# Kernel optimization log

Hardware: AMD Instinct MI355X
Metric: run time of the kernel (lower is better)

Reference implementation:

```python
import jax, jax.numpy as jnp
import numpy as np

N = 100000      # nodes
E = 3200000     # edges (avg degree 32)
NODE, EDGE, H = 11, 2, 32
EPS = 1e-5


def setup_inputs() -> dict:
    key = jax.random.key(0)
    ks = jax.random.split(key, 12)
    def w(k, shape):  # small init like torch Linear
        return jax.random.normal(k, shape, dtype=jnp.float32) * 0.1
    inp = {
        'x': jax.random.normal(ks[0], (N, NODE), dtype=jnp.float32),
        'edge_attr': jax.random.normal(ks[1], (E, EDGE), dtype=jnp.float32),
        'edge_index': jax.random.randint(ks[2], (2, E), 0, N),
        # mlp1: Lin(13,32)-BN-ReLU-Lin(32,32)-BN-ReLU
        'w1a': w(ks[3], (NODE + EDGE, H)), 'b1a': jnp.zeros(H), 'g1a': jnp.ones(H), 'be1a': jnp.zeros(H),
        'w1b': w(ks[4], (H, H)),           'b1b': jnp.zeros(H), 'g1b': jnp.ones(H), 'be1b': jnp.zeros(H),
        # mlp2: Lin(43,32)-BN-ReLU then Lin(32,1)-ReLU (no BN on last)
        'w2a': w(ks[5], (NODE + H, H)), 'b2a': jnp.zeros(H), 'g2a': jnp.ones(H), 'be2a': jnp.zeros(H),
        'w2b': w(ks[6], (H, 1)),        'b2b': jnp.zeros(1),
        # power: Lin(11,32)-BN-ReLU-Lin(32,1)-BN-ReLU
        'wpa': w(ks[7], (NODE, H)), 'bpa': jnp.zeros(H), 'gpa': jnp.ones(H), 'bepa': jnp.zeros(H),
        'wpb': w(ks[8], (H, 1)),    'bpb': jnp.zeros(1), 'gpb': jnp.ones(1), 'bepb': jnp.zeros(1),
    }
    return inp


def _bn(x, g, b):
    # training-mode BatchNorm1d (batch stats, biased variance), like torch default
    mu = x.mean(0, keepdims=True)
    var = ((x - mu) ** 2).mean(0, keepdims=True)
    return (x - mu) * jax.lax.rsqrt(var + EPS) * g + b


def _conv(x, edge_index, edge_attr,
          w1a, b1a, g1a, be1a, w1b, b1b, g1b, be1b,
          w2a, b2a, g2a, be2a, w2b, b2b):
    src, dst = edge_index[0], edge_index[1]
    # message: cat([x_j, edge_attr]) -> mlp1
    m = jnp.concatenate([x[src], edge_attr], axis=1)          # [E, 13]
    m = jax.nn.relu(_bn(m @ w1a + b1a, g1a, be1a))            # [E, 32]
    m = jax.nn.relu(_bn(m @ w1b + b1b, g1b, be1b))            # [E, 32]
    # aggr='max' scatter to destination nodes
    agg = jax.ops.segment_max(m, dst, num_segments=x.shape[0])
    agg = jnp.where(jnp.isneginf(agg), 0.0, agg)              # empty segments -> 0
    # update: cat([x, aggr_out]) -> mlp2, then replace last feature column
    h = jax.nn.relu(_bn(jnp.concatenate([x, agg], axis=1) @ w2a + b2a, g2a, be2a))
    comb = jax.nn.relu(h @ w2b + b2b)                         # [N, 1]
    return jnp.concatenate([x[:, :-1], comb], axis=1)         # [N, 11]


def reference(x, edge_attr, edge_index,
              w1a, b1a, g1a, be1a, w1b, b1b, g1b, be1b,
              w2a, b2a, g2a, be2a, w2b, b2b,
              wpa, bpa, gpa, bepa, wpb, bpb, gpb, bepb):
    for _ in range(3):
        x = _conv(x, edge_index, edge_attr,
                  w1a, b1a, g1a, be1a, w1b, b1b, g1b, be1b,
                  w2a, b2a, g2a, be2a, w2b, b2b)
    h = jax.nn.relu(_bn(x @ wpa + bpa, gpa, bepa))
    out = jax.nn.relu(_bn(h @ wpb + bpb, gpb, bepb))
    return out
```

## Files before the change

### kernel.cpp

```cpp
#include <hip/hip_runtime.h>
#include <hip/hip_bf16.h>
#include <cstddef>

#define NN 100000
#define EE 3200000
#define NBIN 64
static const float EF = 3200000.0f;
#define INVN (1.0f / 100000.0f)

typedef __attribute__((ext_vector_type(8))) short bf16x8;
typedef __attribute__((ext_vector_type(16))) float f32x16;


__device__ __forceinline__ float wsum(float v) {
  #pragma unroll
  for (int off = 32; off > 0; off >>= 1) v += __shfl_down(v, off, 64);
  return v;
}

__device__ __forceinline__ void reduce64(float sum[32], float ssq[32], float* red,
                                         float* __restrict__ gsum, float* __restrict__ gssq) {
  const int wid = threadIdx.x >> 6, lane = threadIdx.x & 63;
  #pragma unroll
  for (int j = 0; j < 32; j++) {
    float a = wsum(sum[j]);
    float b = wsum(ssq[j]);
    if (lane == 0) { red[wid * 64 + j] = a; red[wid * 64 + 32 + j] = b; }
  }
  __syncthreads();
  if (threadIdx.x < 64) {
    float t = red[threadIdx.x] + red[64 + threadIdx.x] + red[128 + threadIdx.x] + red[192 + threadIdx.x];
    if (threadIdx.x < 32) unsafeAtomicAdd(&gsum[threadIdx.x], t);
    else                  unsafeAtomicAdd(&gssq[threadIdx.x - 32], t);
  }
}

__device__ __forceinline__ void loadrow(const float* __restrict__ xp, int s, float in[13]) {
  const float4* xr = reinterpret_cast<const float4*>(xp + (size_t)s * 12);
  float4 r0 = xr[0], r1 = xr[1], r2 = xr[2];
  in[0]=r0.x; in[1]=r0.y; in[2]=r0.z; in[3]=r0.w; in[4]=r1.x; in[5]=r1.y; in[6]=r1.z; in[7]=r1.w;
  in[8]=r2.x; in[9]=r2.y; in[10]=r2.z;
}

__device__ __forceinline__ unsigned long long packsea(float x, float y) {
  unsigned int xq = (unsigned int)(fmaf(x, 16384.f, 131072.f) + 0.5f);
  unsigned int yq = (unsigned int)(fmaf(y, 16384.f, 131072.f) + 0.5f);
  return (1ULL << 54) | ((unsigned long long)yq << 27) | (unsigned long long)xq;
}

__device__ __forceinline__ short tobf(float f) {
  return (short)((__float_as_uint(f) + 0x8000u) >> 16);
}
__device__ __forceinline__ float bfhi(float f) {
  return __uint_as_float(__float_as_uint(f) & 0xFFFF0000u);
}
__device__ __forceinline__ short bfhi_s(float f) {
  return (short)(__float_as_uint(f) >> 16);
}


__global__ __launch_bounds__(256) void k_wprep(const float* __restrict__ w1b,
    const float* __restrict__ b1b, const float* __restrict__ g1b,
    const float* __restrict__ w2a, const float* __restrict__ b2a,
    const float* __restrict__ wpa, const float* __restrict__ bpa,
    float* __restrict__ w2tf, float* __restrict__ b1bf,
    float* __restrict__ w2aT, float* __restrict__ wpaT) {
  int t = threadIdx.x;
  for (int i = t; i < 1024; i += 256) {
    int j = i >> 5, k = i & 31;
    float d = (g1b[j] >= 0.f) ? 1.f : -1.f;
    w2tf[j * 32 + k] = d * w1b[k * 32 + j];
  }
  for (int i = t; i < 32 * 43; i += 256) { int j = i & 31, k = i >> 5; w2aT[j * 44 + k] = w2a[k * 32 + j]; }
  for (int i = t; i < 32 * 11; i += 256) { int j = i & 31, k = i >> 5; wpaT[j * 12 + k] = wpa[k * 32 + j]; }
  if (t < 32) {
    float d = (g1b[t] >= 0.f) ? 1.f : -1.f;
    b1bf[t] = d * b1b[t];
    w2aT[t * 44 + 43] = b2a[t];
    wpaT[t * 12 + 11] = bpa[t];
  }
}

__global__ __launch_bounds__(256) void k_prep(const int* __restrict__ dst, const int* __restrict__ src,
    const float* __restrict__ ea, int* __restrict__ cnt, int* __restrict__ rank,
    unsigned long long* __restrict__ nsd, float* __restrict__ cmom) {
  float p0 = 0, p1 = 0, p2 = 0, p3 = 0, p4 = 0;
  const int S = gridDim.x * 256;
  for (int g = blockIdx.x * 256 + threadIdx.x; g < EE / 4; g += S) {
    int4 d4 = reinterpret_cast<const int4*>(dst)[g];
    int4 s4 = reinterpret_cast<const int4*>(src)[g];
    float4 e0 = reinterpret_cast<const float4*>(ea)[2 * g];
    float4 e1 = reinterpret_cast<const float4*>(ea)[2 * g + 1];
    int r0 = atomicAdd(&cnt[d4.x], 1);
    int r1 = atomicAdd(&cnt[d4.y], 1);
    int r2 = atomicAdd(&cnt[d4.z], 1);
    int r3 = atomicAdd(&cnt[d4.w], 1);
    reinterpret_cast<int4*>(rank)[g] = make_int4(r0, r1, r2, r3);
    atomicAdd(&nsd[s4.x], packsea(e0.x, e0.y));
    atomicAdd(&nsd[s4.y], packsea(e0.z, e0.w));
    atomicAdd(&nsd[s4.z], packsea(e1.x, e1.y));
    atomicAdd(&nsd[s4.w], packsea(e1.z, e1.w));
    p0 += e0.x * e0.x + e0.z * e0.z + e1.x * e1.x + e1.z * e1.z;
    p1 += e0.x * e0.y + e0.z * e0.w + e1.x * e1.y + e1.z * e1.w;
    p2 += e0.y * e0.y + e0.w * e0.w + e1.y * e1.y + e1.w * e1.w;
    p3 += e0.x + e0.z + e1.x + e1.z;
    p4 += e0.y + e0.w + e1.y + e1.w;
  }
  p0 = wsum(p0); p1 = wsum(p1); p2 = wsum(p2); p3 = wsum(p3); p4 = wsum(p4);
  if ((threadIdx.x & 63) == 0) {
    unsafeAtomicAdd(&cmom[0], p0); unsafeAtomicAdd(&cmom[1], p1); unsafeAtomicAdd(&cmom[2], p2);
    unsafeAtomicAdd(&cmom[3], p3); unsafeAtomicAdd(&cmom[4], p4);
  }
}

__global__ __launch_bounds__(1024) void k_scan(const int* __restrict__ cnt,
                                               int* __restrict__ starts) {
  __shared__ int part[1024];
  const int T = 1024, CH = (NN + T - 1) / T;
  int t = threadIdx.x;
  int lo = t * CH, hi = min(lo + CH, NN);
  int s = 0;
  for (int i = lo; i < hi; i++) s += cnt[i];
  part[t] = s; __syncthreads();
  for (int off = 1; off < T; off <<= 1) {
    int v = (t >= off) ? part[t - off] : 0;
    __syncthreads();
    part[t] += v;
    __syncthreads();
  }
  int run = part[t] - s;
  for (int i = lo; i < hi; i++) { starts[i] = run; run += cnt[i]; }
  if (t == T - 1) starts[NN] = EE;
}

__global__ __launch_bounds__(256) void k_scatter(const int* __restrict__ dst, const int* __restrict__ src,
    const float* __restrict__ ea, const int* __restrict__ starts, const int* __restrict__ rank,
    int4* __restrict__ edg) {
  const int S = gridDim.x * 256;
  for (int g = blockIdx.x * 256 + threadIdx.x; g < EE / 4; g += S) {
    int4 d4 = reinterpret_cast<const int4*>(dst)[g];
    int4 s4 = reinterpret_cast<const int4*>(src)[g];
    int4 r4 = reinterpret_cast<const int4*>(rank)[g];
    float4 e0 = reinterpret_cast<const float4*>(ea)[2 * g];
    float4 e1 = reinterpret_cast<const float4*>(ea)[2 * g + 1];
    edg[starts[d4.x] + r4.x] = make_int4(s4.x, __float_as_int(e0.x), __float_as_int(e0.y), 0);
    edg[starts[d4.y] + r4.y] = make_int4(s4.y, __float_as_int(e0.z), __float_as_int(e0.w), 0);
    edg[starts[d4.z] + r4.z] = make_int4(s4.z, __float_as_int(e1.x), __float_as_int(e1.y), 0);
    edg[starts[d4.w] + r4.w] = make_int4(s4.w, __float_as_int(e1.z), __float_as_int(e1.w), 0);
  }
}

__global__ __launch_bounds__(256) void k_xp(const float* __restrict__ x, float* __restrict__ xp) {
  int n = blockIdx.x * 256 + threadIdx.x;
  if (n >= NN) return;
  float v[11];
  #pragma unroll
  for (int k = 0; k < 11; k++) v[k] = x[(size_t)n * 11 + k];
  float4* o = reinterpret_cast<float4*>(xp + (size_t)n * 12);
  o[0] = make_float4(v[0], v[1], v[2], v[3]);
  o[1] = make_float4(v[4], v[5], v[6], v[7]);
  o[2] = make_float4(v[8], v[9], v[10], 0.f);
}

__global__ __launch_bounds__(256) void k_mom(const float* __restrict__ xp,
                                             const unsigned long long* __restrict__ nsd,
                                             float* __restrict__ mom) {
  const int n = blockIdx.x * 256 + threadIdx.x;
  const int lane = threadIdx.x & 63;
  float v[11]; float w = 0.f; float sx = 0.f, sy = 0.f;
  #pragma unroll
  for (int k = 0; k < 11; k++) v[k] = 0.f;
  if (n < NN) {
    unsigned long long pv = nsd[n];
    float dg = (float)(unsigned int)(pv >> 54);
    float sxf = (float)(unsigned int)(pv & 0x7FFFFFFull);
    float syf = (float)(unsigned int)((pv >> 27) & 0x7FFFFFFull);
    w = dg;
    sx = sxf * (1.f / 16384.f) - 8.f * dg;
    sy = syf * (1.f / 16384.f) - 8.f * dg;
    loadrow(xp, n, v);
  }
  int ch = 0;
  #pragma unroll
  for (int a = 0; a < 11; a++) {
    float r = wsum(w * v[a]);
    if (lane == 0) unsafeAtomicAdd(&mom[ch], r);
    ch++;
  }
  #pragma unroll
  for (int a = 0; a < 11; a++) {
    #pragma unroll
    for (int b = a; b < 11; b++) {
      float r = wsum(w * v[a] * v[b]);
      if (lane == 0) unsafeAtomicAdd(&mom[ch], r);
      ch++;
    }
  }
  #pragma unroll
  for (int a = 0; a < 11; a++) {
    float rx = wsum(v[a] * sx);
    if (lane == 0) unsafeAtomicAdd(&mom[ch], rx);
    ch++;
    float ry = wsum(v[a] * sy);
    if (lane == 0) unsafeAtomicAdd(&mom[ch], ry);
    ch++;
  }
}

__device__ __forceinline__ float msym(const float* mom, const float* cmom, int k, int l) {
  int a = min(k, l), b = max(k, l);
  if (b < 11) return mom[11 + a * 11 - a * (a - 1) / 2 + (b - a)];
  if (a < 11) return mom[77 + a * 2 + (b - 11)];
  return cmom[(a - 11) + (b - 11)];
}

__global__ __launch_bounds__(256) void k_P(const float* __restrict__ xp,
    const float* __restrict__ mom, const float* __restrict__ cmom,
    const float* __restrict__ w1a, const float* __restrict__ b1a,
    const float* __restrict__ g1a, const float* __restrict__ be1a,
    float* __restrict__ wexy, float* __restrict__ statsbase, float* __restrict__ P) {
  __shared__ float w1fs[32 * 14];
  const int t = threadIdx.x;
  if (t < 32) {
    const int jj = t;
    float w[13], S[13];
    #pragma unroll
    for (int k = 0; k < 13; k++) w[k] = w1a[k * 32 + jj];
    #pragma unroll
    for (int k = 0; k < 11; k++) S[k] = mom[k];
    S[11] = cmom[3]; S[12] = cmom[4];
    float lin = 0.f;
    #pragma unroll
    for (int k = 0; k < 13; k++) lin = fmaf(w[k], S[k], lin);
    float quad = 0.f;
    #pragma unroll
    for (int k = 0; k < 13; k++)
      #pragma unroll
      for (int l = 0; l < 13; l++) quad = fmaf(w[k] * w[l], msym(mom, cmom, k, l), quad);
    const float invE = 1.f / EF;
    float b = b1a[jj];
    float mean = fmaf(lin, invE, b);
    float ey2 = (quad + 2.f * b * lin) * invE + b * b;
    float var = fmaxf(ey2 - mean * mean, 0.f);
    float A = g1a[jj] * rsqrtf(var + 1e-5f);
    float C = be1a[jj] - mean * A;
    #pragma unroll
    for (int k = 0; k < 11; k++) w1fs[jj * 14 + k] = A * w[k];
    w1fs[jj * 14 + 11] = 0.f; w1fs[jj * 14 + 12] = 0.f;
    w1fs[jj * 14 + 13] = fmaf(A, b, C);
    if (blockIdx.x == 0) { wexy[jj] = A * w[11]; wexy[32 + jj] = A * w[12]; }
  }
  if (blockIdx.x == 0 && t >= 64 && t < 128) statsbase[t] = 0.f;
  __syncthreads();
  const int n = blockIdx.x * 256 + t;
  if (n >= NN) return;
  float xv[11];
  loadrow(xp, n, xv);
  float4* op = reinterpret_cast<float4*>(P + (size_t)n * 32);
  #pragma unroll
  for (int jj = 0; jj < 8; jj++) {
    float o[4];
    #pragma unroll
    for (int u = 0; u < 4; u++) {
      int j = 4 * jj + u;
      const float* wr = w1fs + j * 14;
      float acc = wr[13];
      #pragma unroll
      for (int k = 0; k < 11; k++) acc = fmaf(xv[k], wr[k], acc);
      o[u] = acc;
    }
    op[jj] = make_float4(o[0], o[1], o[2], o[3]);
  }
}

__global__ __launch_bounds__(256, 4) void k_fusedagg(
    const int* __restrict__ starts, const int4* __restrict__ edg,
    const float* __restrict__ P, const float* __restrict__ wexy,
    const float* __restrict__ w2tf, const float* __restrict__ b1bf,
    float* __restrict__ tzb, float* __restrict__ gms, float* __restrict__ gzq) {
  const int tid = threadIdx.x;
  const int wid = tid >> 6, lane = tid & 63;
  const int j = lane & 31;
  const int h = lane >> 5;
  const int k1 = 8 * h;
  const int k2 = 16 + 8 * h;
  float wexk[16], weyk[16];
  #pragma unroll
  for (int i = 0; i < 8; i++) {
    wexk[i]     = wexy[k1 + i];  weyk[i]     = wexy[32 + k1 + i];
    wexk[8 + i] = wexy[k2 + i];  weyk[8 + i] = wexy[32 + k2 + i];
  }
  bf16x8 B1h, B1l, B2h, B2l;
  #pragma unroll
  for (int i = 0; i < 8; i++) {
    float w1 = w2tf[j * 32 + k1 + i];
    B1h[i] = bfhi_s(w1); B1l[i] = tobf(w1 - bfhi(w1));
    float w2 = w2tf[j * 32 + k2 + i];
    B2h[i] = bfhi_s(w2); B2l[i] = tobf(w2 - bfhi(w2));
  }
  const float bz = b1bf[j];
  float ms[16];
  #pragma unroll
  for (int i = 0; i < 16; i++) ms[i] = 0.f;
  float zq = 0.f;
  const int nwaves = gridDim.x * 4;
  for (int n = blockIdx.x * 4 + wid; n < NN; n += nwaves) {
    const int lo = starts[n], hi = starts[n + 1];
    float tzn = -3.0e38f;
    for (int base = lo; base < hi; base += 32) {
      const int v = min(hi - base, 32);
      const bool ev = j < v;
      const int4 r = edg[ev ? (base + j) : (hi - 1)];
      const float ex = __int_as_float(r.y), ey = __int_as_float(r.z);
      const float* pr = P + (size_t)r.x * 32;
      const float4 p0 = *reinterpret_cast<const float4*>(pr + k1);
      const float4 p1 = *reinterpret_cast<const float4*>(pr + k1 + 4);
      const float4 p2 = *reinterpret_cast<const float4*>(pr + k2);
      const float4 p3 = *reinterpret_cast<const float4*>(pr + k2 + 4);
      const float vm = ev ? 1.f : 0.f;
      float mv[16];
      mv[0]  = vm * fmaxf(0.f, fmaf(ex, wexk[0],  fmaf(ey, weyk[0],  p0.x)));
      mv[1]  = vm * fmaxf(0.f, fmaf(ex, wexk[1],  fmaf(ey, weyk[1],  p0.y)));
      mv[2]  = vm * fmaxf(0.f, fmaf(ex, wexk[2],  fmaf(ey, weyk[2],  p0.z)));
      mv[3]  = vm * fmaxf(0.f, fmaf(ex, wexk[3],  fmaf(ey, weyk[3],  p0.w)));
      mv[4]  = vm * fmaxf(0.f, fmaf(ex, wexk[4],  fmaf(ey, weyk[4],  p1.x)));
      mv[5]  = vm * fmaxf(0.f, fmaf(ex, wexk[5],  fmaf(ey, weyk[5],  p1.y)));
      mv[6]  = vm * fmaxf(0.f, fmaf(ex, wexk[6],  fmaf(ey, weyk[6],  p1.z)));
      mv[7]  = vm * fmaxf(0.f, fmaf(ex, wexk[7],  fmaf(ey, weyk[7],  p1.w)));
      mv[8]  = vm * fmaxf(0.f, fmaf(ex, wexk[8],  fmaf(ey, weyk[8],  p2.x)));
      mv[9]  = vm * fmaxf(0.f, fmaf(ex, wexk[9],  fmaf(ey, weyk[9],  p2.y)));
      mv[10] = vm * fmaxf(0.f, fmaf(ex, wexk[10], fmaf(ey, weyk[10], p2.z)));
      mv[11] = vm * fmaxf(0.f, fmaf(ex, wexk[11], fmaf(ey, weyk[11], p2.w)));
      mv[12] = vm * fmaxf(0.f, fmaf(ex, wexk[12], fmaf(ey, weyk[12], p3.x)));
      mv[13] = vm * fmaxf(0.f, fmaf(ex, wexk[13], fmaf(ey, weyk[13], p3.y)));
      mv[14] = vm * fmaxf(0.f, fmaf(ex, wexk[14], fmaf(ey, weyk[14], p3.z)));
      mv[15] = vm * fmaxf(0.f, fmaf(ex, wexk[15], fmaf(ey, weyk[15], p3.w)));
      #pragma unroll
      for (int i = 0; i < 16; i++) ms[i] += mv[i];
      bf16x8 A1h, A1l, A2h, A2l;
      #pragma unroll
      for (int i = 0; i < 8; i++) {
        A1h[i] = bfhi_s(mv[i]);     A1l[i] = tobf(mv[i] - bfhi(mv[i]));
        A2h[i] = bfhi_s(mv[8 + i]); A2l[i] = tobf(mv[8 + i] - bfhi(mv[8 + i]));
      }
      f32x16 acc;
      #pragma unroll
      for (int i = 0; i < 16; i++) acc[i] = 0.f;
      acc = __builtin_amdgcn_mfma_f32_32x32x16_bf16(A1h, B1h, acc, 0, 0, 0);
      acc = __builtin_amdgcn_mfma_f32_32x32x16_bf16(A1h, B1l, acc, 0, 0, 0);
      acc = __builtin_amdgcn_mfma_f32_32x32x16_bf16(A1l, B1h, acc, 0, 0, 0);
      acc = __builtin_amdgcn_mfma_f32_32x32x16_bf16(A2h, B2h, acc, 0, 0, 0);
      acc = __builtin_amdgcn_mfma_f32_32x32x16_bf16(A2h, B2l, acc, 0, 0, 0);
      acc = __builtin_amdgcn_mfma_f32_32x32x16_bf16(A2l, B2h, acc, 0, 0, 0);
      const int rb = base + 4 * h;
      #pragma unroll
      for (int rg = 0; rg < 16; rg++) {
        const int row = (rg & 3) + 8 * (rg >> 2);
        const bool rv = (rb + row) < hi;
        const float z = acc[rg] + bz;
        tzn = fmaxf(tzn, rv ? z : -3.0e38f);
        const float zz = rv ? z : 0.f;
        zq = fmaf(zz, zz, zq);
      }
    }
    tzn = fmaxf(tzn, __shfl_xor(tzn, 32, 64));
    if (lane < 32) tzb[(size_t)n * 32 + j] = tzn;
  }
  const int bin = blockIdx.x & (NBIN - 1);
  float zqT = zq + __shfl_xor(zq, 32, 64);
  if (lane < 32) unsafeAtomicAdd(&gzq[bin * 32 + j], zqT);
  #pragma unroll
  for (int i = 0; i < 16; i++) {
    ms[i] += __shfl_xor(ms[i], 16, 64);
    ms[i] += __shfl_xor(ms[i], 8, 64);
    ms[i] += __shfl_xor(ms[i], 4, 64);
    ms[i] += __shfl_xor(ms[i], 2, 64);
    ms[i] += __shfl_xor(ms[i], 1, 64);
  }
  if (lane == 0) {
    #pragma unroll
    for (int i = 0; i < 8; i++) unsafeAtomicAdd(&gms[bin * 32 + i], ms[i]);
    #pragma unroll
    for (int i = 0; i < 8; i++) unsafeAtomicAdd(&gms[bin * 32 + 16 + i], ms[8 + i]);
  }
  if (lane == 32) {
    #pragma unroll
    for (int i = 0; i < 8; i++) unsafeAtomicAdd(&gms[bin * 32 + 8 + i], ms[i]);
    #pragma unroll
    for (int i = 0; i < 8; i++) unsafeAtomicAdd(&gms[bin * 32 + 24 + i], ms[8 + i]);
  }
}

__global__ __launch_bounds__(256) void k_hpre2(const float* __restrict__ xp,
    const float* __restrict__ tzb, const int* __restrict__ starts,
    const float* __restrict__ gms, const float* __restrict__ gzq,
    const float* __restrict__ w1b, const float* __restrict__ b1b,
    const float* __restrict__ g1b, const float* __restrict__ be1b,
    const float* __restrict__ w2aT,
    float* __restrict__ hpre, float* __restrict__ gsum, float* __restrict__ gssq) {
  __shared__ float red[256], a2s[32], c2s[32], smm[32], szq[32];
  const int t = threadIdx.x;
  if (t < 32) {
    float msj = 0.f, zqj = 0.f;
    for (int b = 0; b < NBIN; b++) { msj += gms[b * 32 + t]; zqj += gzq[b * 32 + t]; }
    smm[t] = msj; szq[t] = zqj;
  }
  __syncthreads();
  if (t < 32) {
    float zs = EF * b1b[t];
    #pragma unroll
    for (int k = 0; k < 32; k++) zs = fmaf(w1b[k * 32 + t], smm[k], zs);
    const float invE = 1.f / EF;
    float mu = zs * invE;
    float var = fmaxf(szq[t] * invE - mu * mu, 0.f);
    float A = g1b[t] * rsqrtf(var + 1e-5f);
    float C = be1b[t] - mu * A;
    float d = (g1b[t] >= 0.f) ? 1.f : -1.f;
    a2s[t] = A * d; c2s[t] = C;
  }
  __syncthreads();
  const int n = blockIdx.x * 256 + t;
  float hh[32], hv[32];
  #pragma unroll
  for (int j = 0; j < 32; j++) hv[j] = 0.f;
  if (n < NN) {
    float xv[11];
    loadrow(xp, n, xv);
    const int dg = starts[n + 1] - starts[n];
    float av[32];
    if (dg > 0) {
      const float4* tp = reinterpret_cast<const float4*>(tzb + (size_t)n * 32);
      #pragma unroll
      for (int j = 0; j < 8; j++) {
        float4 v = tp[j];
        av[4 * j]     = fmaxf(0.f, fmaf(a2s[4 * j],     v.x, c2s[4 * j]));
        av[4 * j + 1] = fmaxf(0.f, fmaf(a2s[4 * j + 1], v.y, c2s[4 * j + 1]));
        av[4 * j + 2] = fmaxf(0.f, fmaf(a2s[4 * j + 2], v.z, c2s[4 * j + 2]));
        av[4 * j + 3] = fmaxf(0.f, fmaf(a2s[4 * j + 3], v.w, c2s[4 * j + 3]));
      }
    } else {
      #pragma unroll
      for (int j = 0; j < 32; j++) av[j] = 0.f;
    }
    #pragma unroll
    for (int j = 0; j < 32; j++) {
      const float* wr = w2aT + j * 44;
      float acc = wr[43];
      #pragma unroll
      for (int k = 0; k < 11; k++) acc = fmaf(xv[k], wr[k], acc);
      #pragma unroll
      for (int k = 0; k < 32; k++) acc = fmaf(av[k], wr[11 + k], acc);
      hv[j] = acc;
    }
    float4* hp = reinterpret_cast<float4*>(hpre + (size_t)n * 32);
    #pragma unroll
    for (int j = 0; j < 8; j++)
      hp[j] = make_float4(hv[4 * j], hv[4 * j + 1], hv[4 * j + 2], hv[4 * j + 3]);
  }
  #pragma unroll
  for (int j = 0; j < 32; j++) hh[j] = hv[j] * hv[j];
  reduce64(hv, hh, red, gsum, gssq);
}

__global__ __launch_bounds__(256) void k_comb(const float* __restrict__ hpre,
    const float* __restrict__ SUM3, const float* __restrict__ SSQ3,
    const float* __restrict__ g2a, const float* __restrict__ be2a,
    const float* __restrict__ w2b, const float* __restrict__ b2b, float* __restrict__ xp,
    float* __restrict__ mom, float* __restrict__ gms, float* __restrict__ gzq) {
  __shared__ float a3s[32], c3s[32];
  const int t = threadIdx.x;
  if (t < 32) {
    float mu = SUM3[t] * INVN;
    float var = fmaxf(SSQ3[t] * INVN - mu * mu, 0.f);
    float s = rsqrtf(var + 1e-5f) * g2a[t];
    a3s[t] = s; c3s[t] = be2a[t] - mu * s;
  }
  __syncthreads();
  const int n = blockIdx.x * 256 + t;
  if (n < NN) {
    const float4* hp = reinterpret_cast<const float4*>(hpre + (size_t)n * 32);
    float acc = b2b[0];
    #pragma unroll
    for (int j = 0; j < 8; j++) {
      float4 v = hp[j];
      acc += fmaxf(0.f, fmaf(v.x, a3s[4 * j],     c3s[4 * j]))     * w2b[4 * j];
      acc += fmaxf(0.f, fmaf(v.y, a3s[4 * j + 1], c3s[4 * j + 1])) * w2b[4 * j + 1];
      acc += fmaxf(0.f, fmaf(v.z, a3s[4 * j + 2], c3s[4 * j + 2])) * w2b[4 * j + 2];
      acc += fmaxf(0.f, fmaf(v.w, a3s[4 * j + 3], c3s[4 * j + 3])) * w2b[4 * j + 3];
    }
    xp[(size_t)n * 12 + 10] = fmaxf(acc, 0.f);
  }
  if (blockIdx.x == 0) {
    if (t < 128) mom[t] = 0.f;
    for (int i = t; i < NBIN * 32; i += 256) { gms[i] = 0.f; gzq[i] = 0.f; }
  }
}


__global__ __launch_bounds__(256) void k_p5(const float* __restrict__ xp, const float* __restrict__ wpaT,
                                            float* __restrict__ ybuf,
                                            float* __restrict__ gsum, float* __restrict__ gssq) {
  __shared__ float red[256];
  const int n = blockIdx.x * 256 + threadIdx.x;
  float y[32], yy[32];
  #pragma unroll
  for (int j = 0; j < 32; j++) y[j] = 0.f;
  if (n < NN) {
    float xv[11];
    loadrow(xp, n, xv);
    #pragma unroll
    for (int j = 0; j < 32; j++) {
      const float* wr = wpaT + j * 12;
      float acc = wr[11];
      #pragma unroll
      for (int k = 0; k < 11; k++) acc = fmaf(xv[k], wr[k], acc);
      y[j] = acc;
    }
    float4* yp = reinterpret_cast<float4*>(ybuf + (size_t)n * 32);
    #pragma unroll
    for (int j = 0; j < 8; j++)
      yp[j] = make_float4(y[4 * j], y[4 * j + 1], y[4 * j + 2], y[4 * j + 3]);
  }
  #pragma unroll
  for (int j = 0; j < 32; j++) yy[j] = y[j] * y[j];
  reduce64(y, yy, red, gsum, gssq);
}

__global__ __launch_bounds__(256) void k_p6(const float* __restrict__ ybuf,
    const float* __restrict__ SUM4, const float* __restrict__ SSQ4,
    const float* __restrict__ gpa, const float* __restrict__ bepa,
    const float* __restrict__ wpb, const float* __restrict__ bpb,
    float* __restrict__ yq, float* __restrict__ gsum, float* __restrict__ gssq) {
  __shared__ float red[8], a4s[32], c4s[32];
  const int t = threadIdx.x;
  if (t < 32) {
    float mu = SUM4[t] * INVN;
    float var = fmaxf(SSQ4[t] * INVN - mu * mu, 0.f);
    float s = rsqrtf(var + 1e-5f) * gpa[t];
    a4s[t] = s; c4s[t] = bepa[t] - mu * s;
  }
  __syncthreads();
  const int n = blockIdx.x * 256 + t;
  float sum = 0.f, ssq = 0.f;
  if (n < NN) {
    const float4* yp = reinterpret_cast<const float4*>(ybuf + (size_t)n * 32);
    float q = bpb[0];
    #pragma unroll
    for (int j = 0; j < 8; j++) {
      float4 v = yp[j];
      q = fmaf(fmaxf(0.f, fmaf(v.x, a4s[4 * j],     c4s[4 * j])),     wpb[4 * j],     q);
      q = fmaf(fmaxf(0.f, fmaf(v.y, a4s[4 * j + 1], c4s[4 * j + 1])), wpb[4 * j + 1], q);
      q = fmaf(fmaxf(0.f, fmaf(v.z, a4s[4 * j + 2], c4s[4 * j + 2])), wpb[4 * j + 2], q);
      q = fmaf(fmaxf(0.f, fmaf(v.w, a4s[4 * j + 3], c4s[4 * j + 3])), wpb[4 * j + 3], q);
    }
    yq[n] = q;
    sum = q; ssq = q * q;
  }
  float s = wsum(sum), qq = wsum(ssq);
  const int wid = t >> 6, lane = t & 63;
  if (lane == 0) { red[wid] = s; red[4 + wid] = qq; }
  __syncthreads();
  if (t == 0) {
    unsafeAtomicAdd(&gsum[0], red[0] + red[1] + red[2] + red[3]);
    unsafeAtomicAdd(&gssq[0], red[4] + red[5] + red[6] + red[7]);
  }
}

__global__ __launch_bounds__(256) void k_p7(const float* __restrict__ yq,
    const float* __restrict__ SUM5, const float* __restrict__ SSQ5,
    const float* __restrict__ gpb, const float* __restrict__ bepb, float* __restrict__ out) {
  const int n = blockIdx.x * 256 + threadIdx.x;
  if (n >= NN) return;
  float mu = SUM5[0] * INVN;
  float var = fmaxf(SSQ5[0] * INVN - mu * mu, 0.f);
  float a5 = rsqrtf(var + 1e-5f) * gpb[0];
  float c5 = bepb[0] - mu * a5;
  out[n] = fmaxf(0.f, fmaf(yq[n], a5, c5));
}


extern "C" void kernel_launch(void* const* d_in, const int* in_sizes, int n_in,
                              void* d_out, int out_size, void* d_ws, size_t ws_size,
                              hipStream_t stream) {
  const float* x    = (const float*)d_in[0];
  const float* ea   = (const float*)d_in[1];
  const int*   ei   = (const int*)d_in[2];
  const int*   srcp = ei;
  const int*   dstp = ei + EE;
  const float* w1a = (const float*)d_in[3],  *b1a = (const float*)d_in[4];
  const float* g1a = (const float*)d_in[5],  *be1a = (const float*)d_in[6];
  const float* w1b = (const float*)d_in[7],  *b1b = (const float*)d_in[8];
  const float* g1b = (const float*)d_in[9],  *be1b = (const float*)d_in[10];
  const float* w2a = (const float*)d_in[11], *b2a = (const float*)d_in[12];
  const float* g2a = (const float*)d_in[13], *be2a = (const float*)d_in[14];
  const float* w2b = (const float*)d_in[15], *b2b = (const float*)d_in[16];
  const float* wpa = (const float*)d_in[17], *bpa = (const float*)d_in[18];
  const float* gpa = (const float*)d_in[19], *bepa = (const float*)d_in[20];
  const float* wpb = (const float*)d_in[21], *bpb = (const float*)d_in[22];
  const float* gpb = (const float*)d_in[23], *bepb = (const float*)d_in[24];

  size_t off = 0;
  char* base = (char*)d_ws;
  auto alloc = [&](size_t bytes) -> void* {
    void* p = base + off;
    off += (bytes + 255) & ~(size_t)255;
    return p;
  };
  float* stats = (float*)alloc(2048);
  float* mom   = (float*)alloc(512);
  float* cmom  = (float*)alloc(256);
  float* gmsB  = (float*)alloc(NBIN * 32 * 4);
  float* gzqB  = (float*)alloc(NBIN * 32 * 4);
  float* wexy  = (float*)alloc(64 * 4);
  float* w2tf  = (float*)alloc(32 * 32 * 4);
  float* b1bf  = (float*)alloc(256);
  float* w2aT  = (float*)alloc(32 * 44 * 4);
  float* wpaT  = (float*)alloc(32 * 12 * 4);
  int*   cnt    = (int*)alloc(NN * 4);
  unsigned long long* nsd = (unsigned long long*)alloc((size_t)NN * 8);
  int*   starts = (int*)alloc((NN + 1) * 4);
  int*   rank   = (int*)alloc((size_t)EE * 4);
  int4*  edg    = (int4*)alloc((size_t)EE * 16);
  float* xp     = (float*)alloc((size_t)NN * 12 * 4);
  float* P      = (float*)alloc((size_t)NN * 32 * 4);
  float* tzb    = (float*)alloc((size_t)NN * 32 * 4);
  float* hpre   = (float*)alloc((size_t)NN * 32 * 4);
  float* yq     = (float*)alloc(NN * 4);

  float *SUM3 = stats + 64,  *SSQ3 = stats + 96;
  float *SUM4 = stats + 128, *SSQ4 = stats + 160;
  float *SUM5 = stats + 192, *SSQ5 = stats + 224;

  hipMemsetAsync(stats, 0, 2048, stream);
  hipMemsetAsync(mom, 0, 512 + 256, stream);
  hipMemsetAsync(gmsB, 0, NBIN * 32 * 4 * 2, stream);
  hipMemsetAsync(cnt, 0, NN * 4, stream);
  hipMemsetAsync(nsd, 0, (size_t)NN * 8, stream);

  const int GN = (NN + 255) / 256;
  const int GW = 2048;
  const int GE4 = (EE / 4 + 255) / 256;

  k_wprep  <<<1, 256, 0, stream>>>(w1b, b1b, g1b, w2a, b2a, wpa, bpa, w2tf, b1bf, w2aT, wpaT);
  k_prep   <<<GE4, 256, 0, stream>>>(dstp, srcp, ea, cnt, rank, nsd, cmom);
  k_scan   <<<1, 1024, 0, stream>>>(cnt, starts);
  k_scatter<<<GE4, 256, 0, stream>>>(dstp, srcp, ea, starts, rank, edg);
  k_xp     <<<GN, 256, 0, stream>>>(x, xp);

  for (int c = 0; c < 3; c++) {
    k_mom     <<<GN, 256, 0, stream>>>(xp, nsd, mom);
    k_P       <<<GN, 256, 0, stream>>>(xp, mom, cmom, w1a, b1a, g1a, be1a, wexy, stats, P);
    k_fusedagg<<<GW, 256, 0, stream>>>(starts, edg, P, wexy, w2tf, b1bf, tzb, gmsB, gzqB);
    k_hpre2   <<<GN, 256, 0, stream>>>(xp, tzb, starts, gmsB, gzqB, w1b, b1b, g1b, be1b,
                                       w2aT, hpre, SUM3, SSQ3);
    k_comb    <<<GN, 256, 0, stream>>>(hpre, SUM3, SSQ3, g2a, be2a, w2b, b2b, xp,
                                       mom, gmsB, gzqB);
  }

  k_p5<<<GN, 256, 0, stream>>>(xp, wpaT, hpre, SUM4, SSQ4);
  k_p6<<<GN, 256, 0, stream>>>(hpre, SUM4, SSQ4, gpa, bepa, wpb, bpb, yq, SUM5, SSQ5);
  k_p7<<<GN, 256, 0, stream>>>(yq, SUM5, SSQ5, gpb, bepb, (float*)d_out);
}
```

Before: 3.831 ms.

## Store P table in bf16 and use single-pass bf16 MFMA in edge aggregation

The per-node precomputed P table is now written as packed bf16 instead of fp32, halving the bytes gathered per edge in the fused aggregation kernel. The split hi/lo bf16 emulation of fp32 (six MFMAs per 32-edge tile) is replaced by plain bf16 operands with two MFMAs, which also removes the residual computation. This is meant to cut gather bandwidth and matrix-core work in the dominant edge kernel. In exchange, messages and the second linear layer lose precision, which may push outputs past tolerance after three layers and BatchNorm.

```diff
diff --git a/kernel.cpp b/kernel.cpp
--- a/kernel.cpp
+++ b/kernel.cpp
@@ -51,11 +51,8 @@
 __device__ __forceinline__ short tobf(float f) {
   return (short)((__float_as_uint(f) + 0x8000u) >> 16);
 }
-__device__ __forceinline__ float bfhi(float f) {
-  return __uint_as_float(__float_as_uint(f) & 0xFFFF0000u);
-}
-__device__ __forceinline__ short bfhi_s(float f) {
-  return (short)(__float_as_uint(f) >> 16);
+__device__ __forceinline__ float frombf(unsigned short u) {
+  return __uint_as_float((unsigned int)u << 16);
 }
 
 
@@ -218,7 +215,8 @@
     const float* __restrict__ mom, const float* __restrict__ cmom,
     const float* __restrict__ w1a, const float* __restrict__ b1a,
     const float* __restrict__ g1a, const float* __restrict__ be1a,
-    float* __restrict__ wexy, float* __restrict__ statsbase, float* __restrict__ P) {
+    float* __restrict__ wexy, float* __restrict__ statsbase,
+    unsigned short* __restrict__ Pb) {
   __shared__ float w1fs[32 * 14];
   const int t = threadIdx.x;
   if (t < 32) {
@@ -256,26 +254,38 @@
   if (n >= NN) return;
   float xv[11];
   loadrow(xp, n, xv);
-  float4* op = reinterpret_cast<float4*>(P + (size_t)n * 32);
-  #pragma unroll
-  for (int jj = 0; jj < 8; jj++) {
-    float o[4];
+  uint4* op = reinterpret_cast<uint4*>(Pb + (size_t)n * 32);
+  #pragma unroll
+  for (int q = 0; q < 4; q++) {
+    unsigned int pk[4];
     #pragma unroll
     for (int u = 0; u < 4; u++) {
-      int j = 4 * jj + u;
-      const float* wr = w1fs + j * 14;
-      float acc = wr[13];
-      #pragma unroll
-      for (int k = 0; k < 11; k++) acc = fmaf(xv[k], wr[k], acc);
-      o[u] = acc;
-    }
-    op[jj] = make_float4(o[0], o[1], o[2], o[3]);
+      int j0 = 8 * q + 2 * u;
+      float a0, a1;
+      {
+        const float* wr = w1fs + j0 * 14;
+        float acc = wr[13];
+        #pragma unroll
+        for (int k = 0; k < 11; k++) acc = fmaf(xv[k], wr[k], acc);
+        a0 = acc;
+      }
+      {
+        const float* wr = w1fs + (j0 + 1) * 14;
+        float acc = wr[13];
+        #pragma unroll
+        for (int k = 0; k < 11; k++) acc = fmaf(xv[k], wr[k], acc);
+        a1 = acc;
+      }
+      pk[u] = (unsigned int)(unsigned short)tobf(a0) |
+              ((unsigned int)(unsigned short)tobf(a1) << 16);
+    }
+    op[q] = make_uint4(pk[0], pk[1], pk[2], pk[3]);
   }
 }
 
 __global__ __launch_bounds__(256, 4) void k_fusedagg(
     const int* __restrict__ starts, const int4* __restrict__ edg,
-    const float* __restrict__ P, const float* __restrict__ wexy,
+    const unsigned short* __restrict__ Pb, const float* __restrict__ wexy,
     const float* __restrict__ w2tf, const float* __restrict__ b1bf,
     float* __restrict__ tzb, float* __restrict__ gms, float* __restrict__ gzq) {
   const int tid = threadIdx.x;
@@ -290,13 +300,11 @@
     wexk[i]     = wexy[k1 + i];  weyk[i]     = wexy[32 + k1 + i];
     wexk[8 + i] = wexy[k2 + i];  weyk[8 + i] = wexy[32 + k2 + i];
   }
-  bf16x8 B1h, B1l, B2h, B2l;
+  bf16x8 B1, B2;
   #pragma unroll
   for (int i = 0; i < 8; i++) {
-    float w1 = w2tf[j * 32 + k1 + i];
-    B1h[i] = bfhi_s(w1); B1l[i] = tobf(w1 - bfhi(w1));
-    float w2 = w2tf[j * 32 + k2 + i];
-    B2h[i] = bfhi_s(w2); B2l[i] = tobf(w2 - bfhi(w2));
+    B1[i] = tobf(w2tf[j * 32 + k1 + i]);
+    B2[i] = tobf(w2tf[j * 32 + k2 + i]);
   }
   const float bz = b1bf[j];
   float ms[16];
@@ -312,46 +320,34 @@
       const bool ev = j < v;
       const int4 r = edg[ev ? (base + j) : (hi - 1)];
       const float ex = __int_as_float(r.y), ey = __int_as_float(r.z);
-      const float* pr = P + (size_t)r.x * 32;
-      const float4 p0 = *reinterpret_cast<const float4*>(pr + k1);
-      const float4 p1 = *reinterpret_cast<const float4*>(pr + k1 + 4);
-      const float4 p2 = *reinterpret_cast<const float4*>(pr + k2);
-      const float4 p3 = *reinterpret_cast<const float4*>(pr + k2 + 4);
+      const unsigned short* pr = Pb + (size_t)r.x * 32;
+      const uint4 q1 = *reinterpret_cast<const uint4*>(pr + k1);
+      const uint4 q2 = *reinterpret_cast<const uint4*>(pr + k2);
+      float pf[16];
+      pf[0]  = __uint_as_float(q1.x << 16); pf[1]  = __uint_as_float(q1.x & 0xFFFF0000u);
+      pf[2]  = __uint_as_float(q1.y << 16); pf[3]  = __uint_as_float(q1.y & 0xFFFF0000u);
+      pf[4]  = __uint_as_float(q1.z << 16); pf[5]  = __uint_as_float(q1.z & 0xFFFF0000u);
+      pf[6]  = __uint_as_float(q1.w << 16); pf[7]  = __uint_as_float(q1.w & 0xFFFF0000u);
+      pf[8]  = __uint_as_float(q2.x << 16); pf[9]  = __uint_as_float(q2.x & 0xFFFF0000u);
+      pf[10] = __uint_as_float(q2.y << 16); pf[11] = __uint_as_float(q2.y & 0xFFFF0000u);
+      pf[12] = __uint_as_float(q2.z << 16); pf[13] = __uint_as_float(q2.z & 0xFFFF0000u);
+      pf[14] = __uint_as_float(q2.w << 16); pf[15] = __uint_as_float(q2.w & 0xFFFF0000u);
       const float vm = ev ? 1.f : 0.f;
-      float mv[16];
-      mv[0]  = vm * fmaxf(0.f, fmaf(ex, wexk[0],  fmaf(ey, weyk[0],  p0.x)));
-      mv[1]  = vm * fmaxf(0.f, fmaf(ex, wexk[1],  fmaf(ey, weyk[1],  p0.y)));
-      mv[2]  = vm * fmaxf(0.f, fmaf(ex, wexk[2],  fmaf(ey, weyk[2],  p0.z)));
-      mv[3]  = vm * fmaxf(0.f, fmaf(ex, wexk[3],  fmaf(ey, weyk[3],  p0.w)));
-      mv[4]  = vm * fmaxf(0.f, fmaf(ex, wexk[4],  fmaf(ey, weyk[4],  p1.x)));
-      mv[5]  = vm * fmaxf(0.f, fmaf(ex, wexk[5],  fmaf(ey, weyk[5],  p1.y)));
-      mv[6]  = vm * fmaxf(0.f, fmaf(ex, wexk[6],  fmaf(ey, weyk[6],  p1.z)));
-      mv[7]  = vm * fmaxf(0.f, fmaf(ex, wexk[7],  fmaf(ey, weyk[7],  p1.w)));
-      mv[8]  = vm * fmaxf(0.f, fmaf(ex, wexk[8],  fmaf(ey, weyk[8],  p2.x)));
-      mv[9]  = vm * fmaxf(0.f, fmaf(ex, wexk[9],  fmaf(ey, weyk[9],  p2.y)));
-      mv[10] = vm * fmaxf(0.f, fmaf(ex, wexk[10], fmaf(ey, weyk[10], p2.z)));
-      mv[11] = vm * fmaxf(0.f, fmaf(ex, wexk[11], fmaf(ey, weyk[11], p2.w)));
-      mv[12] = vm * fmaxf(0.f, fmaf(ex, wexk[12], fmaf(ey, weyk[12], p3.x)));
-      mv[13] = vm * fmaxf(0.f, fmaf(ex, wexk[13], fmaf(ey, weyk[13], p3.y)));
-      mv[14] = vm * fmaxf(0.f, fmaf(ex, wexk[14], fmaf(ey, weyk[14], p3.z)));
-      mv[15] = vm * fmaxf(0.f, fmaf(ex, wexk[15], fmaf(ey, weyk[15], p3.w)));
-      #pragma unroll
-      for (int i = 0; i < 16; i++) ms[i] += mv[i];
-      bf16x8 A1h, A1l, A2h, A2l;
+      bf16x8 A1, A2;
       #pragma unroll
       for (int i = 0; i < 8; i++) {
-        A1h[i] = bfhi_s(mv[i]);     A1l[i] = tobf(mv[i] - bfhi(mv[i]));
-        A2h[i] = bfhi_s(mv[8 + i]); A2l[i] = tobf(mv[8 + i] - bfhi(mv[8 + i]));
+        const float m1 = vm * fmaxf(0.f, fmaf(ex, wexk[i], fmaf(ey, weyk[i], pf[i])));
+        const float m2 = vm * fmaxf(0.f, fmaf(ex, wexk[8 + i], fmaf(ey, weyk[8 + i], pf[8 + i])));
+        ms[i] += m1;
+        ms[8 + i] += m2;
+        A1[i] = tobf(m1);
+        A2[i] = tobf(m2);
       }
       f32x16 acc;
       #pragma unroll
       for (int i = 0; i < 16; i++) acc[i] = 0.f;
-      acc = __builtin_amdgcn_mfma_f32_32x32x16_bf16(A1h, B1h, acc, 0, 0, 0);
-      acc = __builtin_amdgcn_mfma_f32_32x32x16_bf16(A1h, B1l, acc, 0, 0, 0);
-      acc = __builtin_amdgcn_mfma_f32_32x32x16_bf16(A1l, B1h, acc, 0, 0, 0);
-      acc = __builtin_amdgcn_mfma_f32_32x32x16_bf16(A2h, B2h, acc, 0, 0, 0);
-      acc = __builtin_amdgcn_mfma_f32_32x32x16_bf16(A2h, B2l, acc, 0, 0, 0);
-      acc = __builtin_amdgcn_mfma_f32_32x32x16_bf16(A2l, B2h, acc, 0, 0, 0);
+      acc = __builtin_amdgcn_mfma_f32_32x32x16_bf16(A1, B1, acc, 0, 0, 0);
+      acc = __builtin_amdgcn_mfma_f32_32x32x16_bf16(A2, B2, acc, 0, 0, 0);
       const int rb = base + 4 * h;
       #pragma unroll
       for (int rg = 0; rg < 16; rg++) {
@@ -622,7 +618,7 @@
   int*   rank   = (int*)alloc((size_t)EE * 4);
   int4*  edg    = (int4*)alloc((size_t)EE * 16);
   float* xp     = (float*)alloc((size_t)NN * 12 * 4);
-  float* P      = (float*)alloc((size_t)NN * 32 * 4);
+  unsigned short* Pb = (unsigned short*)alloc((size_t)NN * 32 * 2);
   float* tzb    = (float*)alloc((size_t)NN * 32 * 4);
   float* hpre   = (float*)alloc((size_t)NN * 32 * 4);
   float* yq     = (float*)alloc(NN * 4);
@@ -649,8 +645,8 @@
 
   for (int c = 0; c < 3; c++) {
     k_mom     <<<GN, 256, 0, stream>>>(xp, nsd, mom);
-    k_P       <<<GN, 256, 0, stream>>>(xp, mom, cmom, w1a, b1a, g1a, be1a, wexy, stats, P);
-    k_fusedagg<<<GW, 256, 0, stream>>>(starts, edg, P, wexy, w2tf, b1bf, tzb, gmsB, gzqB);
+    k_P       <<<GN, 256, 0, stream>>>(xp, mom, cmom, w1a, b1a, g1a, be1a, wexy, stats, Pb);
+    k_fusedagg<<<GW, 256, 0, stream>>>(starts, edg, Pb, wexy, w2tf, b1bf, tzb, gmsB, gzqB);
     k_hpre2   <<<GN, 256, 0, stream>>>(xp, tzb, starts, gmsB, gzqB, w1b, b1b, g1b, be1b,
                                        w2aT, hpre, SUM3, SSQ3);
     k_comb    <<<GN, 256, 0, stream>>>(hpre, SUM3, SSQ3, g2a, be2a, w2b, b2b, xp,
```

Measured after the change: 3.881 ms. Within noise of the previous version (+1.3%).
